# Kernel tuning notes

Hardware: AMD Instinct MI355X
Metric: run time of the kernel (lower is better)

The kernel has to match this reference:

```python
import jax, jax.numpy as jnp
import numpy as np


def _gru_direction(x_lin, h0, w_hh, b_hh, hidden):
    """Run GRU recurrence over time for one direction.
    x_lin: [S, B, 3H] precomputed input projection (W_ih @ x + b_ih)
    h0: [B, H]; w_hh: [3H, H]; b_hh: [3H]. Returns [S, B, H]."""
    H = hidden

    def step(h, gx):
        gh = jnp.einsum('bh,gh->bg', h, w_hh) + b_hh  # [B, 3H]
        r = jax.nn.sigmoid(gx[:, :H] + gh[:, :H])
        z = jax.nn.sigmoid(gx[:, H:2 * H] + gh[:, H:2 * H])
        n = jnp.tanh(gx[:, 2 * H:] + r * gh[:, 2 * H:])
        h_new = (1.0 - z) * n + z * h
        return h_new, h_new

    _, out = jax.lax.scan(step, h0, x_lin)
    return out


def setup_inputs() -> dict:
    key = jax.random.key(0)
    ks = jax.random.split(key, 7)
    S, B, I, H, L = 512, 64, 1024, 1024, 3
    stdv = 1.0 / np.sqrt(H)
    x = jax.random.normal(ks[0], (S, B, I), dtype=jnp.float32)
    h0 = jax.random.normal(ks[1], (L * 2, B, H), dtype=jnp.float32)
    w_ih0 = jax.random.uniform(ks[2], (2, 3 * H, I), minval=-stdv, maxval=stdv, dtype=jnp.float32)
    w_ih = jax.random.uniform(ks[3], (L - 1, 2, 3 * H, 2 * H), minval=-stdv, maxval=stdv, dtype=jnp.float32)
    w_hh = jax.random.uniform(ks[4], (L, 2, 3 * H, H), minval=-stdv, maxval=stdv, dtype=jnp.float32)
    b_ih = jax.random.uniform(ks[5], (L, 2, 3 * H), minval=-stdv, maxval=stdv, dtype=jnp.float32)
    b_hh = jax.random.uniform(ks[6], (L, 2, 3 * H), minval=-stdv, maxval=stdv, dtype=jnp.float32)
    return {"x": x, "h0": h0, "w_ih0": w_ih0, "w_ih": w_ih,
            "w_hh": w_hh, "b_ih": b_ih, "b_hh": b_hh}


def reference(x, h0, w_ih0, w_ih, w_hh, b_ih, b_hh):
    L = w_hh.shape[0]
    H = w_hh.shape[-1]
    layer_input = x  # [S, B, in]
    for layer in range(L):
        dir_outs = []
        for d in range(2):
            Wih = w_ih0[d] if layer == 0 else w_ih[layer - 1, d]
            xi = layer_input if d == 0 else layer_input[::-1]
            # big input-projection GEMM once per layer/direction
            gx = jnp.einsum('sbi,gi->sbg', xi, Wih) + b_ih[layer, d]
            out = _gru_direction(gx, h0[layer * 2 + d], w_hh[layer, d], b_hh[layer, d], H)
            if d == 1:
                out = out[::-1]
            dir_outs.append(out)
        layer_input = jnp.concatenate(dir_outs, axis=-1)  # [S, B, 2H]
    return layer_input
```

## Files before the change

### kernel.cpp

```cpp
#include <hip/hip_runtime.h>
#include <stdint.h>

typedef uint16_t u16;
typedef __attribute__((ext_vector_type(8))) short bf16x8;
typedef __attribute__((ext_vector_type(4))) float f32x4;
typedef __attribute__((ext_vector_type(4))) unsigned u32x4;

#define DEVI __device__ __forceinline__

DEVI u16 f2b(float f) {
  uint32_t u = __float_as_uint(f);
  uint32_t r = (u + 0x7fffu + ((u >> 16) & 1u)) >> 16;
  return (u16)r;
}
DEVI float b2f(u16 h) { return __uint_as_float(((uint32_t)h) << 16); }

typedef const __attribute__((address_space(1))) uint32_t* gptr_t;
typedef __attribute__((address_space(3))) uint32_t* lptr_t;
DEVI void gload_lds16(const void* g, void* l) {
  __builtin_amdgcn_global_load_lds((gptr_t)g, (lptr_t)l, 16, 0, 0);
}

DEVI bf16x8 ld_cc16(const u16* p) {
  bf16x8 r;
  asm volatile("global_load_dwordx4 %0, %1, off sc0 sc1" : "=v"(r) : "v"(p));
  return r;
}
DEVI void st_cc2(u16* p, u16 v) {
  uint32_t d = v;
  asm volatile("global_store_short %0, %1, off sc0 sc1" :: "v"(p), "v"(d) : "memory");
}
DEVI void st_cc4(unsigned* p, unsigned v) {
  asm volatile("global_store_dword %0, %1, off sc0 sc1" :: "v"(p), "v"(v) : "memory");
}

__global__ void cvt_f32_bf16(const float* __restrict__ in, u16* __restrict__ out, long n) {
  long i = ((long)blockIdx.x * blockDim.x + threadIdx.x) * 4;
  long stride = (long)gridDim.x * blockDim.x * 4;
  for (; i < n; i += stride) {
    float4 v = *(const float4*)(in + i);
    ushort4 o;
    o.x = f2b(v.x); o.y = f2b(v.y); o.z = f2b(v.z); o.w = f2b(v.w);
    *(ushort4*)(out + i) = o;
  }
}

__global__ __launch_bounds__(256) void gemm_bt_bias(
    const u16* __restrict__ A, const u16* __restrict__ W,
    const float* __restrict__ bias, u16* __restrict__ C, int K) {
  constexpr int NLD = 6144;
  __shared__ u16 As[128 * 64];
  __shared__ u16 Bs[128 * 64];
  const int t = threadIdx.x;
  const int l = t & 63, w = t >> 6;
  const int lr = l & 15, lk = l >> 4;
  const long bm = (long)blockIdx.y * 128;
  const long bn = (long)blockIdx.x * 128;
  const int wm = (w >> 1) * 64, wn = (w & 1) * 64;

  f32x4 acc[4][4] = {};

  for (int k0 = 0; k0 < K; k0 += 64) {
    __syncthreads();
    #pragma unroll
    for (int i = 0; i < 4; ++i) {
      int slot = i * 256 + t;
      int row = slot >> 3, s = slot & 7;
      int c8 = (s ^ (row & 7)) * 8;
      char* la = (char*)As + (size_t)(i * 256 + w * 64) * 16;
      char* lb = (char*)Bs + (size_t)(i * 256 + w * 64) * 16;
      gload_lds16(A + (bm + row) * K + k0 + c8, la);
      gload_lds16(W + (bn + row) * K + k0 + c8, lb);
    }
    asm volatile("s_waitcnt vmcnt(0)" ::: "memory");
    __syncthreads();
    #pragma unroll
    for (int kk = 0; kk < 2; ++kk) {
      bf16x8 af[4], bfr[4];
      #pragma unroll
      for (int mi = 0; mi < 4; ++mi) {
        int row = wm + mi * 16 + lr;
        int sl = (kk * 4 + lk) ^ (row & 7);
        af[mi] = *(const bf16x8*)((const char*)As + row * 128 + sl * 16);
      }
      #pragma unroll
      for (int ni = 0; ni < 4; ++ni) {
        int row = wn + ni * 16 + lr;
        int sl = (kk * 4 + lk) ^ (row & 7);
        bfr[ni] = *(const bf16x8*)((const char*)Bs + row * 128 + sl * 16);
      }
      #pragma unroll
      for (int mi = 0; mi < 4; ++mi)
        #pragma unroll
        for (int ni = 0; ni < 4; ++ni)
          acc[mi][ni] = __builtin_amdgcn_mfma_f32_16x16x32_bf16(af[mi], bfr[ni], acc[mi][ni], 0, 0, 0);
    }
  }

  float bv[4];
  #pragma unroll
  for (int ni = 0; ni < 4; ++ni) bv[ni] = bias[bn + wn + ni * 16 + lr];
  #pragma unroll
  for (int mi = 0; mi < 4; ++mi)
    #pragma unroll
    for (int ni = 0; ni < 4; ++ni) {
      long col = bn + wn + ni * 16 + lr;
      #pragma unroll
      for (int j = 0; j < 4; ++j) {
        long row = bm + wm + mi * 16 + lk * 4 + j;
        C[row * NLD + col] = f2b(acc[mi][ni][j] + bv[ni]);
      }
    }
}

DEVI void poll_slots(const unsigned* slots, unsigned tgt, int l) {
  const unsigned* pp = slots + (l & 7) * 4;
  for (;;) {
    u32x4 v;
    asm volatile("global_load_dwordx4 %0, %1, off sc0 sc1" : "=v"(v) : "v"(pp));
    asm volatile("s_waitcnt vmcnt(0)" ::: "memory");
    int ok = (l < 8) ? (v.x >= tgt && v.y >= tgt && v.z >= tgt && v.w >= tgt) : 1;
    if (__all(ok)) break;
    __builtin_amdgcn_s_sleep(1);
  }
}

__global__ __launch_bounds__(512, 2) void gru_layer(
    u16* __restrict__ hbA, u16* __restrict__ hbB,
    const u16* __restrict__ Whh,
    const float* __restrict__ bhh,
    const u16* __restrict__ gx,
    u16* __restrict__ y_b, float* __restrict__ y_f,
    const float* __restrict__ h0l,
    unsigned* bar) {
  __shared__ float lds[8 * 64 * 13];

  const int bid = blockIdx.x;
  const int dmn = bid & 7, m = bid >> 3;
  const int dir = dmn >> 2, rg = dmn & 3;
  const int tid = threadIdx.x;
  const int w2 = tid >> 6, l = tid & 63;
  const int lr = l & 15, lk = l >> 4;
  const int ch = w2 & 1, kh = w2 >> 1;

  unsigned* slots = bar + dmn * 64;

  const int fcol5 = tid & 31, frow = tid >> 5;
  const int colg = m * 32 + fcol5;
  const int growd = rg * 16 + frow;
  const float bhr = bhh[dir * 3072 + colg];
  const float bhz = bhh[dir * 3072 + 1024 + colg];
  const float bhn = bhh[dir * 3072 + 2048 + colg];
  const size_t hoff = (size_t)(dir * 64 + growd) * 1024 + colg;
  float hp = h0l[hoff];
  st_cc2(hbA + hoff, f2b(hp));

  const u16* wb = Whh + ((size_t)(dir * 3072 + m * 32 + ch * 16 + lr)) * 1024 + kh * 256 + lk * 8;
  asm volatile("" : "+v"(wb));
  bf16x8 wr[8], wz[8], wn[8];
  #pragma unroll
  for (int kk = 0; kk < 8; ++kk) {
    wr[kk] = *(const bf16x8*)(wb + kk * 32);
    wz[kk] = *(const bf16x8*)(wb + 1024 * 1024 + kk * 32);
    wn[kk] = *(const bf16x8*)(wb + 2048 * 1024 + kk * 32);
  }
  #pragma unroll
  for (int kk = 0; kk < 8; ++kk)
    asm volatile("" : "+a"(wr[kk]), "+a"(wz[kk]), "+a"(wn[kk]));

  const int tt0 = dir ? 511 : 0;
  long gxp = (long)(tt0 * 64 + growd) * 6144 + (long)dir * 3072 + colg;
  const long gxstep = dir ? -(64 * 6144) : (64 * 6144);
  long yp = (long)(tt0 * 64 + growd) * 2048 + (long)dir * 1024 + colg;
  const long ystep = dir ? -(64 * 2048) : (64 * 2048);

  const u16* apA = hbA + (size_t)(dir * 64 + rg * 16 + lr) * 1024 + kh * 256 + lk * 8;
  const u16* apB = hbB + (size_t)(dir * 64 + rg * 16 + lr) * 1024 + kh * 256 + lk * 8;

  const int lf = ((frow >> 2) << 4) | (fcol5 & 15);
  const int jj = frow & 3;
  const int chf = fcol5 >> 4;

  u16 gcr = gx[gxp], gcz = gx[gxp + 1024], gcn = gx[gxp + 2048];

  asm volatile("s_waitcnt vmcnt(0)" ::: "memory");
  __syncthreads();
  if (tid == 0) st_cc4(slots + m, 1u);
  poll_slots(slots, 1u, l);

  for (int t = 0; t < 512; ++t) {
    const u16* ap = (t & 1) ? apB : apA;
    u16* hb_out = (t & 1) ? hbA : hbB;

    bf16x8 av[8];
    #pragma unroll
    for (int kk = 0; kk < 8; ++kk) av[kk] = ld_cc16(ap + kk * 32);
    asm volatile("s_waitcnt vmcnt(0)" ::: "memory");
    __builtin_amdgcn_sched_barrier(0);

    f32x4 aR = {0.f,0.f,0.f,0.f}, aZ = {0.f,0.f,0.f,0.f}, aN = {0.f,0.f,0.f,0.f};
    #pragma unroll
    for (int kk = 0; kk < 8; ++kk) {
      aR = __builtin_amdgcn_mfma_f32_16x16x32_bf16(av[kk], wr[kk], aR, 0, 0, 0);
      aZ = __builtin_amdgcn_mfma_f32_16x16x32_bf16(av[kk], wz[kk], aZ, 0, 0, 0);
      aN = __builtin_amdgcn_mfma_f32_16x16x32_bf16(av[kk], wn[kk], aN, 0, 0, 0);
    }
    float* myl = lds + (size_t)(w2 * 64 + l) * 13;
    #pragma unroll
    for (int j = 0; j < 4; ++j) { myl[j] = aR[j]; myl[4 + j] = aZ[j]; myl[8 + j] = aN[j]; }
    __syncthreads();

    float ghr = 0.f, ghz = 0.f, ghn = 0.f;
    #pragma unroll
    for (int k2 = 0; k2 < 4; ++k2) {
      const float* pl = lds + (size_t)((k2 * 2 + chf) * 64 + lf) * 13;
      ghr += pl[jj]; ghz += pl[4 + jj]; ghn += pl[8 + jj];
    }
    long gxn_p = gxp + gxstep;
    u16 g2r = gx[gxn_p], g2z = gx[gxn_p + 1024], g2n = gx[gxn_p + 2048];

    float rgt = 1.f / (1.f + __expf(-(b2f(gcr) + ghr + bhr)));
    float zgt = 1.f / (1.f + __expf(-(b2f(gcz) + ghz + bhz)));
    float ngt = tanhf(b2f(gcn) + rgt * (ghn + bhn));
    hp = (1.f - zgt) * ngt + zgt * hp;
    st_cc2(hb_out + hoff, f2b(hp));
    if (y_b) y_b[yp] = f2b(hp);
    else     y_f[yp] = hp;

    asm volatile("s_waitcnt vmcnt(0)" ::: "memory");
    gcr = g2r; gcz = g2z; gcn = g2n; gxp = gxn_p; yp += ystep;

    __syncthreads();
    if (tid == 0) st_cc4(slots + m, (unsigned)(t + 2));
    poll_slots(slots, (unsigned)(t + 2), l);
  }
}

extern "C" void kernel_launch(void* const* d_in, const int* in_sizes, int n_in,
                              void* d_out, int out_size, void* d_ws, size_t ws_size,
                              hipStream_t stream) {
  (void)in_sizes; (void)n_in; (void)out_size; (void)ws_size;
  const float* x     = (const float*)d_in[0];
  const float* h0    = (const float*)d_in[1];
  const float* w_ih0 = (const float*)d_in[2];
  const float* w_ih  = (const float*)d_in[3];
  const float* w_hh  = (const float*)d_in[4];
  const float* b_ih  = (const float*)d_in[5];
  const float* b_hh  = (const float*)d_in[6];
  float* out = (float*)d_out;

  char* p = (char*)d_ws;
  u16* wA    = (u16*)p; p += (size_t)32768 * 2048 * 2;
  u16* wGx   = (u16*)p; p += (size_t)32768 * 6144 * 2;
  u16* wWih0 = (u16*)p; p += (size_t)6144 * 1024 * 2;
  u16* wWih  = (u16*)p; p += (size_t)2 * 6144 * 2048 * 2;
  u16* wWhh  = (u16*)p; p += (size_t)6 * 3072 * 1024 * 2;
  u16* wHb0  = (u16*)p; p += (size_t)2 * 64 * 1024 * 2;
  u16* wHb1  = (u16*)p; p += (size_t)2 * 64 * 1024 * 2;
  unsigned* wBar = (unsigned*)p; p += 4096 * 4;

  cvt_f32_bf16<<<2048, 256, 0, stream>>>(x,     wA,    (long)33554432);
  cvt_f32_bf16<<<2048, 256, 0, stream>>>(w_ih0, wWih0, (long)6291456);
  cvt_f32_bf16<<<2048, 256, 0, stream>>>(w_ih,  wWih,  (long)25165824);
  cvt_f32_bf16<<<2048, 256, 0, stream>>>(w_hh,  wWhh,  (long)18874368);

  for (int layer = 0; layer < 3; ++layer) {
    int K = (layer == 0) ? 1024 : 2048;
    const u16* Wg = (layer == 0) ? wWih0 : (wWih + (size_t)(layer - 1) * 6144 * 2048);
    gemm_bt_bias<<<dim3(48, 256), 256, 0, stream>>>(wA, Wg, b_ih + (size_t)layer * 6144, wGx, K);

    hipMemsetAsync(wBar, 0, 4096 * 4, stream);

    const u16* Whh_l   = wWhh + (size_t)layer * 2 * 3072 * 1024;
    const float* bhh_l = b_hh + (size_t)layer * 6144;
    const float* h0_l  = h0 + (size_t)layer * 131072;
    u16*   yb = (layer < 2) ? wA : nullptr;
    float* yf = (layer < 2) ? nullptr : out;
    gru_layer<<<256, 512, 0, stream>>>(wHb0, wHb1, Whh_l, bhh_l, wGx, yb, yf, h0_l, wBar);
  }
}
```

Measured before the change: 9.075 ms.

## Replace block-level barrier with per-wave flags polled across all waves

Each wave now publishes its own progress flag and polls all 256 flags of its direction/row group (64 lanes × 4 dwords) at the start of each step, removing the end-of-step __syncthreads and the single-thread signal. The gx gate inputs are no longer prefetched one step ahead but loaded together with the hidden-state vector. This is meant to cut the block barrier plus inter-block signalling latency on the serial recurrence path. In exchange each poll reads four times more flag data, and the gx load latency now sits inside the step. The bar workspace layout grows from 64 to 256 slots per group.

```diff
diff --git a/kernel.cpp b/kernel.cpp
--- a/kernel.cpp
+++ b/kernel.cpp
@@ -26,12 +26,24 @@
   asm volatile("global_load_dwordx4 %0, %1, off sc0 sc1" : "=v"(r) : "v"(p));
   return r;
 }
+DEVI unsigned ld_g16(const u16* p) {
+  unsigned r;
+  asm volatile("global_load_ushort %0, %1, off" : "=v"(r) : "v"(p));
+  return r;
+}
 DEVI void st_cc2(u16* p, u16 v) {
   uint32_t d = v;
   asm volatile("global_store_short %0, %1, off sc0 sc1" :: "v"(p), "v"(d) : "memory");
 }
 DEVI void st_cc4(unsigned* p, unsigned v) {
   asm volatile("global_store_dword %0, %1, off sc0 sc1" :: "v"(p), "v"(v) : "memory");
+}
+DEVI void st_y16(u16* p, u16 v) {
+  uint32_t d = v;
+  asm volatile("global_store_short %0, %1, off" :: "v"(p), "v"(d) : "memory");
+}
+DEVI void st_y32(float* p, float v) {
+  asm volatile("global_store_dword %0, %1, off" :: "v"(p), "v"(v) : "memory");
 }
 
 __global__ void cvt_f32_bf16(const float* __restrict__ in, u16* __restrict__ out, long n) {
@@ -113,13 +125,13 @@
     }
 }
 
-DEVI void poll_slots(const unsigned* slots, unsigned tgt, int l) {
-  const unsigned* pp = slots + (l & 7) * 4;
+DEVI void poll_all(const unsigned* slots, unsigned tgt, int l) {
+  const unsigned* pp = slots + l * 4;
   for (;;) {
     u32x4 v;
     asm volatile("global_load_dwordx4 %0, %1, off sc0 sc1" : "=v"(v) : "v"(pp));
     asm volatile("s_waitcnt vmcnt(0)" ::: "memory");
-    int ok = (l < 8) ? (v.x >= tgt && v.y >= tgt && v.z >= tgt && v.w >= tgt) : 1;
+    int ok = (v.x >= tgt && v.y >= tgt && v.z >= tgt && v.w >= tgt);
     if (__all(ok)) break;
     __builtin_amdgcn_s_sleep(1);
   }
@@ -143,7 +155,8 @@
   const int lr = l & 15, lk = l >> 4;
   const int ch = w2 & 1, kh = w2 >> 1;
 
-  unsigned* slots = bar + dmn * 64;
+  unsigned* slots = bar + dmn * 256;
+  unsigned* myslot = slots + m * 8 + w2;
 
   const int fcol5 = tid & 31, frow = tid >> 5;
   const int colg = m * 32 + fcol5;
@@ -181,20 +194,21 @@
   const int jj = frow & 3;
   const int chf = fcol5 >> 4;
 
-  u16 gcr = gx[gxp], gcz = gx[gxp + 1024], gcn = gx[gxp + 2048];
-
   asm volatile("s_waitcnt vmcnt(0)" ::: "memory");
-  __syncthreads();
-  if (tid == 0) st_cc4(slots + m, 1u);
-  poll_slots(slots, 1u, l);
+  if (l == 0) st_cc4(myslot, 1u);
 
   for (int t = 0; t < 512; ++t) {
+    poll_all(slots, (unsigned)(t + 1), l);
+
     const u16* ap = (t & 1) ? apB : apA;
     u16* hb_out = (t & 1) ? hbA : hbB;
 
     bf16x8 av[8];
     #pragma unroll
     for (int kk = 0; kk < 8; ++kk) av[kk] = ld_cc16(ap + kk * 32);
+    unsigned gr = ld_g16(gx + gxp);
+    unsigned gz = ld_g16(gx + gxp + 1024);
+    unsigned gn = ld_g16(gx + gxp + 2048);
     asm volatile("s_waitcnt vmcnt(0)" ::: "memory");
     __builtin_amdgcn_sched_barrier(0);
 
@@ -216,23 +230,17 @@
       const float* pl = lds + (size_t)((k2 * 2 + chf) * 64 + lf) * 13;
       ghr += pl[jj]; ghz += pl[4 + jj]; ghn += pl[8 + jj];
     }
-    long gxn_p = gxp + gxstep;
-    u16 g2r = gx[gxn_p], g2z = gx[gxn_p + 1024], g2n = gx[gxn_p + 2048];
-
-    float rgt = 1.f / (1.f + __expf(-(b2f(gcr) + ghr + bhr)));
-    float zgt = 1.f / (1.f + __expf(-(b2f(gcz) + ghz + bhz)));
-    float ngt = tanhf(b2f(gcn) + rgt * (ghn + bhn));
+    float rgt = 1.f / (1.f + __expf(-(b2f((u16)gr) + ghr + bhr)));
+    float zgt = 1.f / (1.f + __expf(-(b2f((u16)gz) + ghz + bhz)));
+    float ngt = tanhf(b2f((u16)gn) + rgt * (ghn + bhn));
     hp = (1.f - zgt) * ngt + zgt * hp;
     st_cc2(hb_out + hoff, f2b(hp));
-    if (y_b) y_b[yp] = f2b(hp);
-    else     y_f[yp] = hp;
-
-    asm volatile("s_waitcnt vmcnt(0)" ::: "memory");
-    gcr = g2r; gcz = g2z; gcn = g2n; gxp = gxn_p; yp += ystep;
-
-    __syncthreads();
-    if (tid == 0) st_cc4(slots + m, (unsigned)(t + 2));
-    poll_slots(slots, (unsigned)(t + 2), l);
+    if (y_b) st_y16(y_b + yp, f2b(hp));
+    else     st_y32(y_f + yp, hp);
+    gxp += gxstep; yp += ystep;
+
+    asm volatile("s_waitcnt vmcnt(0)" ::: "memory");
+    if (l == 0) st_cc4(myslot, (unsigned)(t + 2));
   }
 }
 
```

Measured after the change: 18.34 ms. 102% more time.

## Replace slot-counter barrier with per-element tagged hidden state flags

Applied to the files above, without the earlier changes.

Removes the per-step counter barrier and its polling. Each hidden value is now stored as a 32-bit word that carries a step tag in the upper 16 bits, and consumers spin directly on the data until every tag matches the expected step. This cuts a store-then-poll round trip and a block-wide sync from each timestep, at the cost of doubling the hidden-state read traffic and adding repacking work. The gx prefetch is also moved after the stores, and a base offset per layer keeps tags unique across launches without re-zeroing.

```diff
diff --git a/kernel.cpp b/kernel.cpp
--- a/kernel.cpp
+++ b/kernel.cpp
@@ -21,17 +21,29 @@
   __builtin_amdgcn_global_load_lds((gptr_t)g, (lptr_t)l, 16, 0, 0);
 }
 
-DEVI bf16x8 ld_cc16(const u16* p) {
-  bf16x8 r;
+DEVI u32x4 ld_cc4x(const unsigned* p) {
+  u32x4 r;
   asm volatile("global_load_dwordx4 %0, %1, off sc0 sc1" : "=v"(r) : "v"(p));
   return r;
 }
-DEVI void st_cc2(u16* p, u16 v) {
-  uint32_t d = v;
-  asm volatile("global_store_short %0, %1, off sc0 sc1" :: "v"(p), "v"(d) : "memory");
-}
 DEVI void st_cc4(unsigned* p, unsigned v) {
   asm volatile("global_store_dword %0, %1, off sc0 sc1" :: "v"(p), "v"(v) : "memory");
+}
+DEVI void st_y16(u16* p, u16 v) {
+  uint32_t d = v;
+  asm volatile("global_store_short %0, %1, off" :: "v"(p), "v"(d) : "memory");
+}
+DEVI void st_y32(float* p, float v) {
+  asm volatile("global_store_dword %0, %1, off" :: "v"(p), "v"(v) : "memory");
+}
+
+DEVI bf16x8 pack8(u32x4 lo, u32x4 hi) {
+  union { bf16x8 v; unsigned u[4]; } r;
+  r.u[0] = (lo.x & 0xFFFFu) | (lo.y << 16);
+  r.u[1] = (lo.z & 0xFFFFu) | (lo.w << 16);
+  r.u[2] = (hi.x & 0xFFFFu) | (hi.y << 16);
+  r.u[3] = (hi.z & 0xFFFFu) | (hi.w << 16);
+  return r.v;
 }
 
 __global__ void cvt_f32_bf16(const float* __restrict__ in, u16* __restrict__ out, long n) {
@@ -113,26 +125,14 @@
     }
 }
 
-DEVI void poll_slots(const unsigned* slots, unsigned tgt, int l) {
-  const unsigned* pp = slots + (l & 7) * 4;
-  for (;;) {
-    u32x4 v;
-    asm volatile("global_load_dwordx4 %0, %1, off sc0 sc1" : "=v"(v) : "v"(pp));
-    asm volatile("s_waitcnt vmcnt(0)" ::: "memory");
-    int ok = (l < 8) ? (v.x >= tgt && v.y >= tgt && v.z >= tgt && v.w >= tgt) : 1;
-    if (__all(ok)) break;
-    __builtin_amdgcn_s_sleep(1);
-  }
-}
-
 __global__ __launch_bounds__(512, 2) void gru_layer(
-    u16* __restrict__ hbA, u16* __restrict__ hbB,
+    unsigned* __restrict__ h32A, unsigned* __restrict__ h32B,
     const u16* __restrict__ Whh,
     const float* __restrict__ bhh,
     const u16* __restrict__ gx,
     u16* __restrict__ y_b, float* __restrict__ y_f,
     const float* __restrict__ h0l,
-    unsigned* bar) {
+    unsigned base) {
   __shared__ float lds[8 * 64 * 13];
 
   const int bid = blockIdx.x;
@@ -142,8 +142,6 @@
   const int w2 = tid >> 6, l = tid & 63;
   const int lr = l & 15, lk = l >> 4;
   const int ch = w2 & 1, kh = w2 >> 1;
-
-  unsigned* slots = bar + dmn * 64;
 
   const int fcol5 = tid & 31, frow = tid >> 5;
   const int colg = m * 32 + fcol5;
@@ -153,7 +151,7 @@
   const float bhn = bhh[dir * 3072 + 2048 + colg];
   const size_t hoff = (size_t)(dir * 64 + growd) * 1024 + colg;
   float hp = h0l[hoff];
-  st_cc2(hbA + hoff, f2b(hp));
+  st_cc4(h32A + hoff, ((base + 1u) << 16) | f2b(hp));
 
   const u16* wb = Whh + ((size_t)(dir * 3072 + m * 32 + ch * 16 + lr)) * 1024 + kh * 256 + lk * 8;
   asm volatile("" : "+v"(wb));
@@ -174,8 +172,8 @@
   long yp = (long)(tt0 * 64 + growd) * 2048 + (long)dir * 1024 + colg;
   const long ystep = dir ? -(64 * 2048) : (64 * 2048);
 
-  const u16* apA = hbA + (size_t)(dir * 64 + rg * 16 + lr) * 1024 + kh * 256 + lk * 8;
-  const u16* apB = hbB + (size_t)(dir * 64 + rg * 16 + lr) * 1024 + kh * 256 + lk * 8;
+  const unsigned* rdA = h32A + (size_t)(dir * 64 + rg * 16 + lr) * 1024 + kh * 256 + lk * 8;
+  const unsigned* rdB = h32B + (size_t)(dir * 64 + rg * 16 + lr) * 1024 + kh * 256 + lk * 8;
 
   const int lf = ((frow >> 2) << 4) | (fcol5 & 15);
   const int jj = frow & 3;
@@ -183,20 +181,37 @@
 
   u16 gcr = gx[gxp], gcz = gx[gxp + 1024], gcn = gx[gxp + 2048];
 
-  asm volatile("s_waitcnt vmcnt(0)" ::: "memory");
-  __syncthreads();
-  if (tid == 0) st_cc4(slots + m, 1u);
-  poll_slots(slots, 1u, l);
-
   for (int t = 0; t < 512; ++t) {
-    const u16* ap = (t & 1) ? apB : apA;
-    u16* hb_out = (t & 1) ? hbA : hbB;
+    const unsigned* rd = (t & 1) ? rdB : rdA;
+    unsigned* wrb = (t & 1) ? h32A : h32B;
+    const unsigned want = base + (unsigned)t + 1u;
 
     bf16x8 av[8];
     #pragma unroll
-    for (int kk = 0; kk < 8; ++kk) av[kk] = ld_cc16(ap + kk * 32);
-    asm volatile("s_waitcnt vmcnt(0)" ::: "memory");
-    __builtin_amdgcn_sched_barrier(0);
+    for (int half = 0; half < 2; ++half) {
+      u32x4 lo[4], hi[4];
+      for (;;) {
+        #pragma unroll
+        for (int q = 0; q < 4; ++q) {
+          lo[q] = ld_cc4x(rd + (half * 4 + q) * 32);
+          hi[q] = ld_cc4x(rd + (half * 4 + q) * 32 + 4);
+        }
+        asm volatile("s_waitcnt vmcnt(0)" ::: "memory");
+        __builtin_amdgcn_sched_barrier(0);
+        unsigned ok = 1u;
+        #pragma unroll
+        for (int q = 0; q < 4; ++q) {
+          ok &= (unsigned)((lo[q].x >> 16) == want) & (unsigned)((lo[q].y >> 16) == want)
+              & (unsigned)((lo[q].z >> 16) == want) & (unsigned)((lo[q].w >> 16) == want)
+              & (unsigned)((hi[q].x >> 16) == want) & (unsigned)((hi[q].y >> 16) == want)
+              & (unsigned)((hi[q].z >> 16) == want) & (unsigned)((hi[q].w >> 16) == want);
+        }
+        if (__all((int)ok)) break;
+        __builtin_amdgcn_s_sleep(2);
+      }
+      #pragma unroll
+      for (int q = 0; q < 4; ++q) av[half * 4 + q] = pack8(lo[q], hi[q]);
+    }
 
     f32x4 aR = {0.f,0.f,0.f,0.f}, aZ = {0.f,0.f,0.f,0.f}, aN = {0.f,0.f,0.f,0.f};
     #pragma unroll
@@ -205,6 +220,7 @@
       aZ = __builtin_amdgcn_mfma_f32_16x16x32_bf16(av[kk], wz[kk], aZ, 0, 0, 0);
       aN = __builtin_amdgcn_mfma_f32_16x16x32_bf16(av[kk], wn[kk], aN, 0, 0, 0);
     }
+    __syncthreads();
     float* myl = lds + (size_t)(w2 * 64 + l) * 13;
     #pragma unroll
     for (int j = 0; j < 4; ++j) { myl[j] = aR[j]; myl[4 + j] = aZ[j]; myl[8 + j] = aN[j]; }
@@ -216,23 +232,19 @@
       const float* pl = lds + (size_t)((k2 * 2 + chf) * 64 + lf) * 13;
       ghr += pl[jj]; ghz += pl[4 + jj]; ghn += pl[8 + jj];
     }
-    long gxn_p = gxp + gxstep;
-    u16 g2r = gx[gxn_p], g2z = gx[gxn_p + 1024], g2n = gx[gxn_p + 2048];
-
     float rgt = 1.f / (1.f + __expf(-(b2f(gcr) + ghr + bhr)));
     float zgt = 1.f / (1.f + __expf(-(b2f(gcz) + ghz + bhz)));
     float ngt = tanhf(b2f(gcn) + rgt * (ghn + bhn));
     hp = (1.f - zgt) * ngt + zgt * hp;
-    st_cc2(hb_out + hoff, f2b(hp));
-    if (y_b) y_b[yp] = f2b(hp);
-    else     y_f[yp] = hp;
-
-    asm volatile("s_waitcnt vmcnt(0)" ::: "memory");
-    gcr = g2r; gcz = g2z; gcn = g2n; gxp = gxn_p; yp += ystep;
-
-    __syncthreads();
-    if (tid == 0) st_cc4(slots + m, (unsigned)(t + 2));
-    poll_slots(slots, (unsigned)(t + 2), l);
+    st_cc4(wrb + hoff, ((base + (unsigned)t + 2u) << 16) | f2b(hp));
+    if (y_b) st_y16(y_b + yp, f2b(hp));
+    else     st_y32(y_f + yp, hp);
+
+    long gxn_p = gxp + gxstep;
+    if (t < 511) {
+      gcr = gx[gxn_p]; gcz = gx[gxn_p + 1024]; gcn = gx[gxn_p + 2048];
+    }
+    gxp = gxn_p; yp += ystep;
   }
 }
 
@@ -255,9 +267,11 @@
   u16* wWih0 = (u16*)p; p += (size_t)6144 * 1024 * 2;
   u16* wWih  = (u16*)p; p += (size_t)2 * 6144 * 2048 * 2;
   u16* wWhh  = (u16*)p; p += (size_t)6 * 3072 * 1024 * 2;
-  u16* wHb0  = (u16*)p; p += (size_t)2 * 64 * 1024 * 2;
-  u16* wHb1  = (u16*)p; p += (size_t)2 * 64 * 1024 * 2;
-  unsigned* wBar = (unsigned*)p; p += 4096 * 4;
+  unsigned* h32A = (unsigned*)p; p += (size_t)2 * 64 * 1024 * 4;
+  unsigned* h32B = (unsigned*)p; p += (size_t)2 * 64 * 1024 * 4;
+
+  hipMemsetAsync(h32A, 0, (size_t)2 * 64 * 1024 * 4, stream);
+  hipMemsetAsync(h32B, 0, (size_t)2 * 64 * 1024 * 4, stream);
 
   cvt_f32_bf16<<<2048, 256, 0, stream>>>(x,     wA,    (long)33554432);
   cvt_f32_bf16<<<2048, 256, 0, stream>>>(w_ih0, wWih0, (long)6291456);
@@ -268,14 +282,13 @@
     int K = (layer == 0) ? 1024 : 2048;
     const u16* Wg = (layer == 0) ? wWih0 : (wWih + (size_t)(layer - 1) * 6144 * 2048);
     gemm_bt_bias<<<dim3(48, 256), 256, 0, stream>>>(wA, Wg, b_ih + (size_t)layer * 6144, wGx, K);
-
-    hipMemsetAsync(wBar, 0, 4096 * 4, stream);
 
     const u16* Whh_l   = wWhh + (size_t)layer * 2 * 3072 * 1024;
     const float* bhh_l = b_hh + (size_t)layer * 6144;
     const float* h0_l  = h0 + (size_t)layer * 131072;
     u16*   yb = (layer < 2) ? wA : nullptr;
     float* yf = (layer < 2) ? nullptr : out;
-    gru_layer<<<256, 512, 0, stream>>>(wHb0, wHb1, Whh_l, bhh_l, wGx, yb, yf, h0_l, wBar);
-  }
-}
+    gru_layer<<<256, 512, 0, stream>>>(h32A, h32B, Whh_l, bhh_l, wGx, yb, yf, h0_l,
+                                       (unsigned)(layer * 1024));
+  }
+}
```

After: 14.73 ms. 1.62x slower.

## Replace input-projection GEMM with 256x256 double-buffered pipelined kernel

Applied to the files above, without the earlier changes.

The input-projection GEMM moves from 128x128 tiles with 256 threads and a single LDS buffer to 256x256 tiles with 512 threads. It uses a double-buffered LDS ring in which the next K-slice is fetched with global_load_lds while MFMAs run on the current one, and raises wave priority during the MFMA bursts. This aims to hide global-load latency, raise data reuse per byte loaded, and cut barrier stalls. The cost is 128KB of LDS per block, which limits occupancy, and a final prefetch that reads past the K range into a buffer that is never consumed. The GRU output stores are also switched to plain inline-asm stores.

```diff
diff --git a/kernel.cpp b/kernel.cpp
--- a/kernel.cpp
+++ b/kernel.cpp
@@ -32,6 +32,13 @@
 }
 DEVI void st_cc4(unsigned* p, unsigned v) {
   asm volatile("global_store_dword %0, %1, off sc0 sc1" :: "v"(p), "v"(v) : "memory");
+}
+DEVI void st_y16(u16* p, u16 v) {
+  uint32_t d = v;
+  asm volatile("global_store_short %0, %1, off" :: "v"(p), "v"(d) : "memory");
+}
+DEVI void st_y32(float* p, float v) {
+  asm volatile("global_store_dword %0, %1, off" :: "v"(p), "v"(v) : "memory");
 }
 
 __global__ void cvt_f32_bf16(const float* __restrict__ in, u16* __restrict__ out, long n) {
@@ -45,72 +52,104 @@
   }
 }
 
-__global__ __launch_bounds__(256) void gemm_bt_bias(
+__global__ __launch_bounds__(512, 2) void gemm256(
     const u16* __restrict__ A, const u16* __restrict__ W,
     const float* __restrict__ bias, u16* __restrict__ C, int K) {
   constexpr int NLD = 6144;
-  __shared__ u16 As[128 * 64];
-  __shared__ u16 Bs[128 * 64];
+  __shared__ u16 As[2][16384];
+  __shared__ u16 Bs[2][16384];
   const int t = threadIdx.x;
   const int l = t & 63, w = t >> 6;
   const int lr = l & 15, lk = l >> 4;
-  const long bm = (long)blockIdx.y * 128;
-  const long bn = (long)blockIdx.x * 128;
-  const int wm = (w >> 1) * 64, wn = (w & 1) * 64;
-
-  f32x4 acc[4][4] = {};
-
-  for (int k0 = 0; k0 < K; k0 += 64) {
-    __syncthreads();
-    #pragma unroll
-    for (int i = 0; i < 4; ++i) {
-      int slot = i * 256 + t;
-      int row = slot >> 3, s = slot & 7;
-      int c8 = (s ^ (row & 7)) * 8;
-      char* la = (char*)As + (size_t)(i * 256 + w * 64) * 16;
-      char* lb = (char*)Bs + (size_t)(i * 256 + w * 64) * 16;
-      gload_lds16(A + (bm + row) * K + k0 + c8, la);
-      gload_lds16(W + (bn + row) * K + k0 + c8, lb);
-    }
-    asm volatile("s_waitcnt vmcnt(0)" ::: "memory");
-    __syncthreads();
-    #pragma unroll
-    for (int kk = 0; kk < 2; ++kk) {
-      bf16x8 af[4], bfr[4];
+  const int wm = w >> 2, wn = w & 3;
+  const long bm = (long)blockIdx.y * 256;
+  const long bn = (long)blockIdx.x * 256;
+
+  f32x4 acc[8][4] = {};
+
+  auto stage_half = [&](const u16* gsrc, char* ldst) {
+    #pragma unroll
+    for (int i = 0; i < 2; ++i) {
+      int slotid = i * 512 + t;
+      int r = slotid >> 3, s = slotid & 7;
+      gload_lds16(gsrc + (long)r * K + ((s ^ (r & 7)) * 8),
+                  ldst + i * 8192 + w * 1024);
+    }
+  };
+
+  stage_half(A + bm * K, (char*)As[0]);
+  stage_half(A + (bm + 128) * K, (char*)As[0] + 16384);
+  stage_half(W + bn * K, (char*)Bs[0]);
+  stage_half(W + (bn + 128) * K, (char*)Bs[0] + 16384);
+
+  const int NI = K >> 7;
+  for (int i = 0; i < NI; ++i) {
+    #pragma unroll
+    for (int kt = 0; kt < 2; ++kt) {
+      asm volatile("s_waitcnt vmcnt(0)" ::: "memory");
+      __builtin_amdgcn_s_barrier();
+
+      const int rb = kt;
+      const int sbuf = kt ^ 1;
+      const long k0s = (long)(2 * i + 1 + kt) * 64;
+
       #pragma unroll
-      for (int mi = 0; mi < 4; ++mi) {
-        int row = wm + mi * 16 + lr;
-        int sl = (kk * 4 + lk) ^ (row & 7);
-        af[mi] = *(const bf16x8*)((const char*)As + row * 128 + sl * 16);
+      for (int mh = 0; mh < 2; ++mh) {
+        bf16x8 af[4][2];
+        #pragma unroll
+        for (int m4 = 0; m4 < 4; ++m4) {
+          int row = wm * 128 + (mh * 4 + m4) * 16 + lr;
+          #pragma unroll
+          for (int kk = 0; kk < 2; ++kk) {
+            int sl = (kk * 4 + lk) ^ (row & 7);
+            af[m4][kk] = *(const bf16x8*)((const char*)As[rb] + row * 128 + sl * 16);
+          }
+        }
+        #pragma unroll
+        for (int nh = 0; nh < 2; ++nh) {
+          bf16x8 bfr[2][2];
+          #pragma unroll
+          for (int n2 = 0; n2 < 2; ++n2) {
+            int row = wn * 64 + (nh * 2 + n2) * 16 + lr;
+            #pragma unroll
+            for (int kk = 0; kk < 2; ++kk) {
+              int sl = (kk * 4 + lk) ^ (row & 7);
+              bfr[n2][kk] = *(const bf16x8*)((const char*)Bs[rb] + row * 128 + sl * 16);
+            }
+          }
+          if (mh == 0) stage_half(A + (bm + nh * 128) * K + k0s, (char*)As[sbuf] + nh * 16384);
+          else         stage_half(W + (bn + nh * 128) * K + k0s, (char*)Bs[sbuf] + nh * 16384);
+
+          __builtin_amdgcn_s_barrier();
+          __builtin_amdgcn_s_setprio(1);
+          #pragma unroll
+          for (int m4 = 0; m4 < 4; ++m4)
+            #pragma unroll
+            for (int n2 = 0; n2 < 2; ++n2)
+              #pragma unroll
+              for (int kk = 0; kk < 2; ++kk)
+                acc[mh * 4 + m4][nh * 2 + n2] = __builtin_amdgcn_mfma_f32_16x16x32_bf16(
+                    af[m4][kk], bfr[n2][kk], acc[mh * 4 + m4][nh * 2 + n2], 0, 0, 0);
+          __builtin_amdgcn_s_setprio(0);
+          __builtin_amdgcn_s_barrier();
+        }
       }
-      #pragma unroll
-      for (int ni = 0; ni < 4; ++ni) {
-        int row = wn + ni * 16 + lr;
-        int sl = (kk * 4 + lk) ^ (row & 7);
-        bfr[ni] = *(const bf16x8*)((const char*)Bs + row * 128 + sl * 16);
-      }
-      #pragma unroll
-      for (int mi = 0; mi < 4; ++mi)
-        #pragma unroll
-        for (int ni = 0; ni < 4; ++ni)
-          acc[mi][ni] = __builtin_amdgcn_mfma_f32_16x16x32_bf16(af[mi], bfr[ni], acc[mi][ni], 0, 0, 0);
-    }
-  }
-
-  float bv[4];
+    }
+  }
+
   #pragma unroll
-  for (int ni = 0; ni < 4; ++ni) bv[ni] = bias[bn + wn + ni * 16 + lr];
-  #pragma unroll
-  for (int mi = 0; mi < 4; ++mi)
-    #pragma unroll
-    for (int ni = 0; ni < 4; ++ni) {
-      long col = bn + wn + ni * 16 + lr;
+  for (int ni = 0; ni < 4; ++ni) {
+    long col = bn + wn * 64 + ni * 16 + lr;
+    float bv = bias[col];
+    #pragma unroll
+    for (int mi = 0; mi < 8; ++mi) {
       #pragma unroll
       for (int j = 0; j < 4; ++j) {
-        long row = bm + wm + mi * 16 + lk * 4 + j;
-        C[row * NLD + col] = f2b(acc[mi][ni][j] + bv[ni]);
+        long row = bm + wm * 128 + mi * 16 + lk * 4 + j;
+        C[row * NLD + col] = f2b(acc[mi][ni][j] + bv);
       }
     }
+  }
 }
 
 DEVI void poll_slots(const unsigned* slots, unsigned tgt, int l) {
@@ -224,8 +263,8 @@
     float ngt = tanhf(b2f(gcn) + rgt * (ghn + bhn));
     hp = (1.f - zgt) * ngt + zgt * hp;
     st_cc2(hb_out + hoff, f2b(hp));
-    if (y_b) y_b[yp] = f2b(hp);
-    else     y_f[yp] = hp;
+    if (y_b) st_y16(y_b + yp, f2b(hp));
+    else     st_y32(y_f + yp, hp);
 
     asm volatile("s_waitcnt vmcnt(0)" ::: "memory");
     gcr = g2r; gcz = g2z; gcn = g2n; gxp = gxn_p; yp += ystep;
@@ -267,7 +306,7 @@
   for (int layer = 0; layer < 3; ++layer) {
     int K = (layer == 0) ? 1024 : 2048;
     const u16* Wg = (layer == 0) ? wWih0 : (wWih + (size_t)(layer - 1) * 6144 * 2048);
-    gemm_bt_bias<<<dim3(48, 256), 256, 0, stream>>>(wA, Wg, b_ih + (size_t)layer * 6144, wGx, K);
+    gemm256<<<dim3(24, 128), 512, 0, stream>>>(wA, Wg, b_ih + (size_t)layer * 6144, wGx, K);
 
     hipMemsetAsync(wBar, 0, 4096 * 4, stream);
 
```

Result: faster. 8.457 ms, median of 2 (-6.8%).
